# Performance work log

Measured on AMD Instinct MI355X. Metric: run time of the kernel, lower is better.

## Reference

```python
import math
import jax, jax.numpy as jnp
import numpy as np

B, T, C = 2, 2048, 1024
N_HEAD = 16
HEAD_DIM = C // N_HEAD


def setup_inputs() -> dict:
    key = jax.random.key(0)
    k1, k2, k3 = jax.random.split(key, 3)
    x = jax.random.normal(k1, (B, T, C), dtype=jnp.float32)
    w_attn = jax.random.normal(k2, (3 * C, C), dtype=jnp.float32) * 0.02
    w_proj = jax.random.normal(k3, (C, C), dtype=jnp.float32) * 0.02
    return {"x": x, "w_attn": w_attn, "w_proj": w_proj}


def _rope_cos_sin(seq_len, dim, dtype):
    inv_freq = 1.0 / (10000.0 ** (jnp.arange(0, dim, 2, dtype=jnp.float32) / dim))
    t = jnp.arange(seq_len, dtype=jnp.float32)
    freqs = jnp.einsum('i,j->ij', t, inv_freq)          # [T, dim/2]
    emb = jnp.concatenate([freqs, freqs], axis=-1)       # [T, dim]
    return jnp.cos(emb).astype(dtype), jnp.sin(emb).astype(dtype)


def _rotate_half(x):
    x1, x2 = jnp.split(x, 2, axis=-1)
    return jnp.concatenate([-x2, x1], axis=-1)


def _apply_rope(x, cos, sin):
    # x: [B, H, T, D]; cos/sin: [T, D] broadcast over batch/head
    return x * cos[None, None] + _rotate_half(x) * sin[None, None]


def reference(x, w_attn, w_proj):
    b, t, c = x.shape
    h, d = N_HEAD, c // N_HEAD
    qkv = x @ w_attn.T                                   # [B, T, 3C]
    q, k, v = jnp.split(qkv, 3, axis=-1)
    q = q.reshape(b, t, h, d).transpose(0, 2, 1, 3)      # [B, H, T, D]
    k = k.reshape(b, t, h, d).transpose(0, 2, 1, 3)
    v = v.reshape(b, t, h, d).transpose(0, 2, 1, 3)
    cos, sin = _rope_cos_sin(t, d, x.dtype)
    q = _apply_rope(q, cos, sin)
    k = _apply_rope(k, cos, sin)
    logits = jnp.einsum('bhqd,bhkd->bhqk', q, k) * (1.0 / math.sqrt(d))
    causal = jnp.tril(jnp.ones((t, t), dtype=bool))
    logits = jnp.where(causal[None, None], logits, jnp.float32(-jnp.inf).astype(logits.dtype))
    att = jax.nn.softmax(logits, axis=-1)                # [B, H, T, T]
    y = jnp.einsum('bhqk,bhkd->bhqd', att, v)            # [B, H, T, D]
    y = y.transpose(0, 2, 1, 3).reshape(b, t, c)
    return y @ w_proj.T
```

## Files before the change

kernel.cpp:

```cpp
#include <hip/hip_runtime.h>
#include <hip/hip_bf16.h>
#include <math.h>

#define B_ 2
#define T_ 2048
#define C_ 1024
#define H_ 16

typedef __bf16 bf16x8 __attribute__((ext_vector_type(8)));
typedef __bf16 bf16x4 __attribute__((ext_vector_type(4)));
typedef float f32x4 __attribute__((ext_vector_type(4)));
typedef float f32x16 __attribute__((ext_vector_type(16)));
typedef unsigned int u32;

#if __has_builtin(__builtin_amdgcn_exp2f)
#define EXP2(x) __builtin_amdgcn_exp2f(x)
#else
#define EXP2(x) exp2f(x)
#endif

__device__ __forceinline__ void gload16(const void* g, void* l) {
    __builtin_amdgcn_global_load_lds(
        (const __attribute__((address_space(1))) void*)g,
        (__attribute__((address_space(3))) void*)l, 16, 0, 0);
}

__device__ __forceinline__ f32x4 mfma16(bf16x8 a, bf16x8 b, f32x4 c) {
    return __builtin_amdgcn_mfma_f32_16x16x32_bf16(a, b, c, 0, 0, 0);
}
__device__ __forceinline__ f32x16 mfma32(bf16x8 a, bf16x8 b, f32x16 c) {
    return __builtin_amdgcn_mfma_f32_32x32x16_bf16(a, b, c, 0, 0, 0);
}

__device__ __forceinline__ u32 cvtpk(float lo, float hi) {
    u32 r;
    asm("v_cvt_pk_bf16_f32 %0, %1, %2" : "=v"(r) : "v"(lo), "v"(hi));
    return r;
}

__device__ __forceinline__ void plane32swap(u32& a, u32& b) {
#if __has_builtin(__builtin_amdgcn_permlane32_swap)
    auto r = __builtin_amdgcn_permlane32_swap(a, b, false, false);
    a = r[0]; b = r[1];
#else
    asm("v_permlane32_swap_b32 %0, %1" : "+v"(a), "+v"(b));
#endif
}

#define SCLQ 0.18033688011112042f
#define NLOG2_10K_32 (-0.4152410118609203f)

__global__ __launch_bounds__(256) void cast_all(const float* __restrict__ x,
                                                const float* __restrict__ wa,
                                                const float* __restrict__ wp,
                                                __bf16* __restrict__ xb,
                                                __bf16* __restrict__ wab,
                                                __bf16* __restrict__ wpb) {
    const int i = blockIdx.x * 256 + threadIdx.x;
    const float* src;
    __bf16* dst;
    int k;
    if (i < 1048576)               { src = x;  dst = xb;  k = i; }
    else if (i < 1048576 + 786432) { src = wa; dst = wab; k = i - 1048576; }
    else                           { src = wp; dst = wpb; k = i - (1048576 + 786432); }
    float4 v = ((const float4*)src)[k];
    bf16x4 o;
    o[0] = (__bf16)v.x; o[1] = (__bf16)v.y; o[2] = (__bf16)v.z; o[3] = (__bf16)v.w;
    ((bf16x4*)dst)[k] = o;
}

__global__ __launch_bounds__(256) void gemm_qkv(const __bf16* __restrict__ A,
                                                const __bf16* __restrict__ Bw,
                                                __bf16* __restrict__ Qb,
                                                __bf16* __restrict__ Kb,
                                                __bf16* __restrict__ Vt) {
    const int tid  = threadIdx.x;
    const int lane = tid & 63;
    const int w    = tid >> 6;
    const int wr = w >> 1, wc = w & 1;
    const int l15 = lane & 15, lg = lane >> 4;
    const int bm = blockIdx.y * 128, bn = blockIdx.x * 128;
    const int K = C_;
    __shared__ __bf16 Asm[128 * 64];
    __shared__ __bf16 Bsm[128 * 64];
    f32x4 acc[4][4] = {};

    for (int kt = 0; kt < K; kt += 64) {
        if (kt) __syncthreads();
#pragma unroll
        for (int it = 0; it < 4; ++it) {
            const int c = it * 256 + tid;
            const int row = c >> 3, cc = (c & 7) * 8;
            gload16(A  + (size_t)(bm + row) * K + kt + cc, Asm + c * 8);
            gload16(Bw + (size_t)(bn + row) * K + kt + cc, Bsm + c * 8);
        }
        __syncthreads();
#pragma unroll
        for (int kk = 0; kk < 64; kk += 32) {
            bf16x8 af[4], bf[4];
#pragma unroll
            for (int i = 0; i < 4; ++i)
                af[i] = *(const bf16x8*)&Asm[(wr * 64 + i * 16 + l15) * 64 + kk + lg * 8];
#pragma unroll
            for (int j = 0; j < 4; ++j)
                bf[j] = *(const bf16x8*)&Bsm[(wc * 64 + j * 16 + l15) * 64 + kk + lg * 8];
#pragma unroll
            for (int i = 0; i < 4; ++i)
#pragma unroll
                for (int j = 0; j < 4; ++j)
                    acc[i][j] = mfma16(af[i], bf[j], acc[i][j]);
        }
    }
    const int region  = bn >> 10;
    const int colbase = (bn & 1023) + wc * 64;
    const int h = colbase >> 6;
    if (region < 2) {
        __bf16* dst = region ? Kb : Qb;
        const float scl = region ? 1.0f : SCLQ;
#pragma unroll
        for (int j = 0; j < 2; ++j) {
            const int d = j * 16 + l15;
            const float invf = exp2f((float)d * NLOG2_10K_32);
#pragma unroll
            for (int i = 0; i < 4; ++i)
#pragma unroll
                for (int r = 0; r < 4; ++r) {
                    const int row = bm + wr * 64 + i * 16 + lg * 4 + r;
                    const int b = row >> 11, t = row & (T_ - 1);
                    float sv, cv;
                    __sincosf((float)t * invf, &sv, &cv);
                    const float v1 = acc[i][j][r], v2 = acc[i][j + 2][r];
                    const float o1 = (v1 * cv - v2 * sv) * scl;
                    const float o2 = (v2 * cv + v1 * sv) * scl;
                    const size_t base = ((size_t)(b * H_ + h) * T_ + t) * 64;
                    dst[base + d]      = (__bf16)o1;
                    dst[base + d + 32] = (__bf16)o2;
                }
        }
    } else {
#pragma unroll
        for (int i = 0; i < 4; ++i)
#pragma unroll
            for (int j = 0; j < 4; ++j) {
                const int vcol = colbase + j * 16 + l15;
                const int hh = vcol >> 6, d = vcol & 63;
                const int row0 = bm + wr * 64 + i * 16 + lg * 4;
                const int b = row0 >> 11, t0 = row0 & (T_ - 1);
                u32 dw[2];
                dw[0] = cvtpk(acc[i][j][0], acc[i][j][1]);
                dw[1] = cvtpk(acc[i][j][2], acc[i][j][3]);
                *(uint64_t*)&Vt[((size_t)(b * H_ + hh) * 64 + d) * T_ + t0] =
                    *(uint64_t*)dw;
            }
    }
}

__global__ __launch_bounds__(256) void gemm_proj(const __bf16* __restrict__ A,
                                                 const __bf16* __restrict__ Bw,
                                                 float* __restrict__ Cp,
                                                 int N, int K) {
    const int tid  = threadIdx.x;
    const int lane = tid & 63;
    const int w    = tid >> 6;
    const int wr = w >> 1, wc = w & 1;
    const int l15 = lane & 15, lg = lane >> 4;
    const int bm = blockIdx.y * 64, bn = blockIdx.x * 128;
    __shared__ __bf16 Asm[64 * 64];
    __shared__ __bf16 Bsm[128 * 64];
    f32x4 acc[2][4] = {};

    for (int kt = 0; kt < K; kt += 64) {
        if (kt) __syncthreads();
#pragma unroll
        for (int it = 0; it < 2; ++it) {
            const int g = it * 256 + tid;
            const int row = g >> 3, cc = (g & 7) * 8;
            gload16(A + (size_t)(bm + row) * K + kt + cc, Asm + g * 8);
        }
#pragma unroll
        for (int it = 0; it < 4; ++it) {
            const int g = it * 256 + tid;
            const int row = g >> 3, cc = (g & 7) * 8;
            gload16(Bw + (size_t)(bn + row) * K + kt + cc, Bsm + g * 8);
        }
        __syncthreads();
#pragma unroll
        for (int kk = 0; kk < 64; kk += 32) {
            bf16x8 af[2], bf[4];
#pragma unroll
            for (int i = 0; i < 2; ++i)
                af[i] = *(const bf16x8*)&Asm[(wr * 32 + i * 16 + l15) * 64 + kk + lg * 8];
#pragma unroll
            for (int j = 0; j < 4; ++j)
                bf[j] = *(const bf16x8*)&Bsm[(wc * 64 + j * 16 + l15) * 64 + kk + lg * 8];
#pragma unroll
            for (int i = 0; i < 2; ++i)
#pragma unroll
                for (int j = 0; j < 4; ++j)
                    acc[i][j] = mfma16(af[i], bf[j], acc[i][j]);
        }
    }
#pragma unroll
    for (int i = 0; i < 2; ++i)
#pragma unroll
        for (int j = 0; j < 4; ++j)
#pragma unroll
            for (int r = 0; r < 4; ++r) {
                const int row = bm + wr * 32 + i * 16 + lg * 4 + r;
                const int col = bn + wc * 64 + j * 16 + l15;
                Cp[(size_t)row * N + col] = acc[i][j][r];
            }
}

__global__ __launch_bounds__(256) void attn_fwd(const __bf16* __restrict__ Qb,
                                                const __bf16* __restrict__ Kb,
                                                const __bf16* __restrict__ Vt,
                                                __bf16* __restrict__ Yatt) {
    const int gid = blockIdx.x;
    const int bh = (gid & 7) * 4 + ((gid >> 3) & 3);
    const int qq = gid >> 5;
    const int qt = (qq < 8) ? (15 - qq) : (qq - 8);
    const int b = bh >> 4, h = bh & 15;
    const int tid = threadIdx.x, lane = tid & 63, w = tid >> 6;
    const int l31 = lane & 31, hi = lane >> 5;
    const int hi4 = hi * 4;
    __shared__ __bf16 Ksm[2][128 * 64];
    __shared__ __bf16 Vsm[2][64 * 128];

    const int Q0 = qt * 128 + w * 32;
    const int qg = Q0 + l31;
    const __bf16* Qp = Qb + ((size_t)bh * T_ + Q0) * 64;
    const __bf16* Kp = Kb + (size_t)bh * T_ * 64;
    const __bf16* Vp = Vt + (size_t)bh * 64 * T_;

    auto STAGE = [&](int j) {
        __bf16* Ks = Ksm[j & 1];
        __bf16* Vs = Vsm[j & 1];
#pragma unroll
        for (int it = 0; it < 4; ++it) {
            const int g = it * 256 + tid;
            const int kr = g >> 3, kc = (g & 7) ^ (kr & 7);
            gload16(Kp + ((size_t)(j * 128 + kr)) * 64 + kc * 8, Ks + g * 8);
            const int vd = g >> 4, vg = (g & 15) ^ (vd & 15);
            gload16(Vp + (size_t)vd * T_ + j * 128 + vg * 8, Vs + g * 8);
        }
    };

    const int jmax = qt + 1;
    STAGE(0);

    bf16x8 qf[4];
#pragma unroll
    for (int ds = 0; ds < 4; ++ds)
        qf[ds] = *(const bf16x8*)&Qp[l31 * 64 + ds * 16 + hi * 8];

    f32x16 ot[2] = {};
    float m_run = -1e30f, l_run = 0.f;

    for (int j = 0; j < jmax; ++j) {
        const int cur = j & 1;
        __builtin_amdgcn_s_barrier();
        if (j + 1 < jmax) {
            STAGE(j + 1);
            asm volatile("s_waitcnt vmcnt(8)" ::: "memory");
        } else {
            asm volatile("s_waitcnt vmcnt(0)" ::: "memory");
        }
        __builtin_amdgcn_s_barrier();
        __builtin_amdgcn_sched_barrier(0);

        f32x16 st[4] = {};
#pragma unroll
        for (int a = 0; a < 4; ++a)
#pragma unroll
            for (int ds = 0; ds < 4; ++ds) {
                const int row = a * 32 + l31;
                const int off = (ds * 32 + hi * 16) ^ ((row & 7) << 4);
                bf16x8 kf = *(const bf16x8*)((const char*)Ksm[cur] + row * 128 + off);
                st[a] = mfma32(kf, qf[ds], st[a]);
            }
        if (j == qt) {
#pragma unroll
            for (int a = 0; a < 4; ++a)
#pragma unroll
                for (int r = 0; r < 16; ++r) {
                    const int kv = j * 128 + a * 32 + (r & 3) + 8 * (r >> 2) + hi4;
                    if (kv > qg) st[a][r] = -1e30f;
                }
        }
        float t8[8];
#pragma unroll
        for (int i = 0; i < 8; ++i)
            t8[i] = fmaxf(fmaxf(fmaxf(st[0][i], st[0][i + 8]),
                                fmaxf(st[1][i], st[1][i + 8])),
                          fmaxf(fmaxf(st[2][i], st[2][i + 8]),
                                fmaxf(st[3][i], st[3][i + 8])));
        float mx = fmaxf(fmaxf(fmaxf(t8[0], t8[1]), fmaxf(t8[2], t8[3])),
                         fmaxf(fmaxf(t8[4], t8[5]), fmaxf(t8[6], t8[7])));
        mx = fmaxf(mx, __shfl_xor(mx, 32));
        if (!__all(mx - m_run <= 10.f)) {
            const float mnew = fmaxf(m_run, mx);
            const float corr = EXP2(m_run - mnew);
            l_run *= corr;
#pragma unroll
            for (int db = 0; db < 2; ++db)
#pragma unroll
                for (int r = 0; r < 16; ++r) ot[db][r] *= corr;
            m_run = mnew;
        }
        float s0 = 0.f, s1 = 0.f;
#pragma unroll
        for (int a = 0; a < 4; ++a)
#pragma unroll
            for (int r = 0; r < 16; ++r) {
                const float e = EXP2(st[a][r] - m_run);
                st[a][r] = e;
                if (r & 1) s1 += e; else s0 += e;
            }
        float rs = s0 + s1;
        rs += __shfl_xor(rs, 32);
        l_run += rs;
        bf16x8 pa[8];
#pragma unroll
        for (int ks = 0; ks < 8; ++ks) {
            const int a = ks >> 1, rb = (ks & 1) * 8;
            u32 X0 = cvtpk(st[a][rb + 0], st[a][rb + 1]);
            u32 X1 = cvtpk(st[a][rb + 2], st[a][rb + 3]);
            u32 Y0 = cvtpk(st[a][rb + 4], st[a][rb + 5]);
            u32 Y1 = cvtpk(st[a][rb + 6], st[a][rb + 7]);
            plane32swap(X0, Y0);
            plane32swap(X1, Y1);
            u32 dw[4] = {X0, X1, Y0, Y1};
            pa[ks] = *(bf16x8*)dw;
        }
#pragma unroll
        for (int ks = 0; ks < 8; ++ks)
#pragma unroll
            for (int db = 0; db < 2; ++db) {
                const int row = db * 32 + l31;
                const int off = ((ks * 2 + hi) ^ (row & 15)) * 16;
                bf16x8 vf = *(const bf16x8*)((const char*)Vsm[cur] + row * 256 + off);
                ot[db] = mfma32(vf, pa[ks], ot[db]);
            }
    }
    const float inv = 1.f / l_run;
    __bf16* Yp = Yatt + ((size_t)(b * T_ + qg)) * C_ + h * 64;
#pragma unroll
    for (int db = 0; db < 2; ++db)
#pragma unroll
        for (int rq = 0; rq < 4; ++rq) {
            const int r = rq * 4;
            u32 dw[2];
            dw[0] = cvtpk(ot[db][r] * inv,     ot[db][r + 1] * inv);
            dw[1] = cvtpk(ot[db][r + 2] * inv, ot[db][r + 3] * inv);
            const int d = db * 32 + 8 * rq + hi4;
            *(uint64_t*)&Yp[d] = *(uint64_t*)dw;
        }
}

extern "C" void kernel_launch(void* const* d_in, const int* in_sizes, int n_in,
                              void* d_out, int out_size, void* d_ws, size_t ws_size,
                              hipStream_t stream) {
    const float* x      = (const float*)d_in[0];
    const float* w_attn = (const float*)d_in[1];
    const float* w_proj = (const float*)d_in[2];
    float* out = (float*)d_out;
    char* ws = (char*)d_ws;

    __bf16* xb  = (__bf16*)(ws);
    __bf16* wab = (__bf16*)(ws + 8388608);
    __bf16* wpb = (__bf16*)(ws + 14680064);
    __bf16* Qb  = (__bf16*)(ws + 16777216);
    __bf16* Kb  = (__bf16*)(ws + 25165824);
    __bf16* Vt  = (__bf16*)(ws + 33554432);
    __bf16* Ya  = (__bf16*)(ws + 41943040);

    cast_all<<<dim3(8192), 256, 0, stream>>>(x, w_attn, w_proj, xb, wab, wpb);

    gemm_qkv<<<dim3(3 * C_ / 128, B_ * T_ / 128), 256, 0, stream>>>(
        xb, wab, Qb, Kb, Vt);

    attn_fwd<<<dim3(16 * 32), 256, 0, stream>>>(Qb, Kb, Vt, Ya);

    gemm_proj<<<dim3(C_ / 128, B_ * T_ / 64), 256, 0, stream>>>(
        Ya, wpb, out, C_, C_);
}
```

Measured before the change: 108.9 us.

## Rewrite QKV GEMM as 256x256 double-buffered swizzled tile kernel with priority hints

The QKV projection GEMM moves from 128x128 tiles with 4 warps and single-buffered LDS to 256x256 tiles with 8 warps. Global-to-LDS loads of the next K-step overlap the MFMA work on the current one, using 128 KB of dynamic shared memory and an XOR-swizzled layout to avoid bank conflicts. s_setprio hints are added around the MFMA blocks in both the GEMM and the attention kernel. The grid shrinks to 12x16=192 blocks, which may underfill the 256 CUs and leaves one block per CU because of the LDS size.

```diff
diff --git a/kernel.cpp b/kernel.cpp
--- a/kernel.cpp
+++ b/kernel.cpp
@@ -69,50 +69,94 @@
     ((bf16x4*)dst)[k] = o;
 }
 
-__global__ __launch_bounds__(256) void gemm_qkv(const __bf16* __restrict__ A,
-                                                const __bf16* __restrict__ Bw,
-                                                __bf16* __restrict__ Qb,
-                                                __bf16* __restrict__ Kb,
-                                                __bf16* __restrict__ Vt) {
-    const int tid  = threadIdx.x;
-    const int lane = tid & 63;
-    const int w    = tid >> 6;
-    const int wr = w >> 1, wc = w & 1;
+__global__ __launch_bounds__(512, 2) void gemm_qkv(const __bf16* __restrict__ A,
+                                                   const __bf16* __restrict__ Bw,
+                                                   __bf16* __restrict__ Qb,
+                                                   __bf16* __restrict__ Kb,
+                                                   __bf16* __restrict__ Vt) {
+    extern __shared__ __bf16 smem[];
+    __bf16* Ah = smem;
+    __bf16* Bh = smem + 2 * 2 * 128 * 64;
+    const int tid = threadIdx.x, lane = tid & 63;
+    const int w = tid >> 6, wm = w >> 2, wn = w & 3;
     const int l15 = lane & 15, lg = lane >> 4;
-    const int bm = blockIdx.y * 128, bn = blockIdx.x * 128;
+    const int bm = blockIdx.y * 256, bn = blockIdx.x * 256;
     const int K = C_;
-    __shared__ __bf16 Asm[128 * 64];
-    __shared__ __bf16 Bsm[128 * 64];
-    f32x4 acc[4][4] = {};
-
-    for (int kt = 0; kt < K; kt += 64) {
-        if (kt) __syncthreads();
-#pragma unroll
-        for (int it = 0; it < 4; ++it) {
-            const int c = it * 256 + tid;
-            const int row = c >> 3, cc = (c & 7) * 8;
-            gload16(A  + (size_t)(bm + row) * K + kt + cc, Asm + c * 8);
-            gload16(Bw + (size_t)(bn + row) * K + kt + cc, Bsm + c * 8);
-        }
-        __syncthreads();
-#pragma unroll
-        for (int kk = 0; kk < 64; kk += 32) {
-            bf16x8 af[4], bf[4];
-#pragma unroll
-            for (int i = 0; i < 4; ++i)
-                af[i] = *(const bf16x8*)&Asm[(wr * 64 + i * 16 + l15) * 64 + kk + lg * 8];
-#pragma unroll
-            for (int j = 0; j < 4; ++j)
-                bf[j] = *(const bf16x8*)&Bsm[(wc * 64 + j * 16 + l15) * 64 + kk + lg * 8];
-#pragma unroll
-            for (int i = 0; i < 4; ++i)
-#pragma unroll
-                for (int j = 0; j < 4; ++j)
-                    acc[i][j] = mfma16(af[i], bf[j], acc[i][j]);
+    f32x4 acc[8][4] = {};
+
+    auto STAGE_A = [&](int t) {
+        __bf16* dst = Ah + (t & 1) * (2 * 128 * 64);
+#pragma unroll
+        for (int q2 = 0; q2 < 4; ++q2) {
+            const int qid = q2 * 512 + tid;
+            const int half = qid >> 10;
+            const int row = (qid >> 3) & 127, g = qid & 7;
+            const int sg = g ^ (row & 7);
+            gload16(A + (size_t)(bm + half * 128 + row) * K + t * 64 + sg * 8,
+                    dst + qid * 8);
+        }
+    };
+    auto STAGE_B = [&](int t) {
+        __bf16* dst = Bh + (t & 1) * (2 * 128 * 64);
+#pragma unroll
+        for (int q2 = 0; q2 < 4; ++q2) {
+            const int qid = q2 * 512 + tid;
+            const int half = qid >> 10;
+            const int row = (qid >> 3) & 127, g = qid & 7;
+            const int sg = g ^ (row & 7);
+            gload16(Bw + (size_t)(bn + half * 128 + row) * K + t * 64 + sg * 8,
+                    dst + qid * 8);
+        }
+    };
+
+    STAGE_A(0); STAGE_B(0);
+    asm volatile("s_waitcnt vmcnt(0)" ::: "memory");
+    __builtin_amdgcn_s_barrier();
+
+    for (int t = 0; t < 16; ++t) {
+        const __bf16* As = Ah + (t & 1) * (2 * 128 * 64) + wm * (128 * 64);
+        const __bf16* Bs = Bh + (t & 1) * (2 * 128 * 64) + (wn >> 1) * (128 * 64);
+#pragma unroll
+        for (int p = 0; p < 4; ++p) {
+            const int rh = p >> 1, ch = p & 1;
+            if (p == 0 && t < 15) STAGE_A(t + 1);
+            if (p == 1 && t < 15) STAGE_B(t + 1);
+            bf16x8 af[4][2], bf[2][2];
+#pragma unroll
+            for (int i2 = 0; i2 < 4; ++i2) {
+                const int row = rh * 64 + i2 * 16 + l15;
+#pragma unroll
+                for (int k2 = 0; k2 < 2; ++k2)
+                    af[i2][k2] = *(const bf16x8*)
+                        &As[row * 64 + ((k2 * 4 + lg) ^ (row & 7)) * 8];
+            }
+#pragma unroll
+            for (int j2 = 0; j2 < 2; ++j2) {
+                const int row = (wn & 1) * 64 + ch * 32 + j2 * 16 + l15;
+#pragma unroll
+                for (int k2 = 0; k2 < 2; ++k2)
+                    bf[j2][k2] = *(const bf16x8*)
+                        &Bs[row * 64 + ((k2 * 4 + lg) ^ (row & 7)) * 8];
+            }
+            __builtin_amdgcn_s_barrier();
+            __builtin_amdgcn_s_setprio(1);
+#pragma unroll
+            for (int k2 = 0; k2 < 2; ++k2)
+#pragma unroll
+                for (int i2 = 0; i2 < 4; ++i2)
+#pragma unroll
+                    for (int j2 = 0; j2 < 2; ++j2)
+                        acc[rh * 4 + i2][ch * 2 + j2] =
+                            mfma16(af[i2][k2], bf[j2][k2],
+                                   acc[rh * 4 + i2][ch * 2 + j2]);
+            __builtin_amdgcn_s_setprio(0);
+            if (p == 3) asm volatile("s_waitcnt vmcnt(0)" ::: "memory");
+            __builtin_amdgcn_s_barrier();
         }
     }
-    const int region  = bn >> 10;
-    const int colbase = (bn & 1023) + wc * 64;
+    const int cb = bn + wn * 64;
+    const int region = cb >> 10;
+    const int colbase = cb & 1023;
     const int h = colbase >> 6;
     if (region < 2) {
         __bf16* dst = region ? Kb : Qb;
@@ -122,33 +166,33 @@
             const int d = j * 16 + l15;
             const float invf = exp2f((float)d * NLOG2_10K_32);
 #pragma unroll
-            for (int i = 0; i < 4; ++i)
+            for (int i = 0; i < 8; ++i)
 #pragma unroll
                 for (int r = 0; r < 4; ++r) {
-                    const int row = bm + wr * 64 + i * 16 + lg * 4 + r;
-                    const int b = row >> 11, t = row & (T_ - 1);
+                    const int row = bm + wm * 128 + i * 16 + lg * 4 + r;
+                    const int b = row >> 11, tt = row & (T_ - 1);
                     float sv, cv;
-                    __sincosf((float)t * invf, &sv, &cv);
+                    __sincosf((float)tt * invf, &sv, &cv);
                     const float v1 = acc[i][j][r], v2 = acc[i][j + 2][r];
                     const float o1 = (v1 * cv - v2 * sv) * scl;
                     const float o2 = (v2 * cv + v1 * sv) * scl;
-                    const size_t base = ((size_t)(b * H_ + h) * T_ + t) * 64;
+                    const size_t base = ((size_t)(b * H_ + h) * T_ + tt) * 64;
                     dst[base + d]      = (__bf16)o1;
                     dst[base + d + 32] = (__bf16)o2;
                 }
         }
     } else {
 #pragma unroll
-        for (int i = 0; i < 4; ++i)
-#pragma unroll
-            for (int j = 0; j < 4; ++j) {
-                const int vcol = colbase + j * 16 + l15;
+        for (int i = 0; i < 8; ++i)
+#pragma unroll
+            for (int jj = 0; jj < 4; ++jj) {
+                const int vcol = colbase + jj * 16 + l15;
                 const int hh = vcol >> 6, d = vcol & 63;
-                const int row0 = bm + wr * 64 + i * 16 + lg * 4;
+                const int row0 = bm + wm * 128 + i * 16 + lg * 4;
                 const int b = row0 >> 11, t0 = row0 & (T_ - 1);
                 u32 dw[2];
-                dw[0] = cvtpk(acc[i][j][0], acc[i][j][1]);
-                dw[1] = cvtpk(acc[i][j][2], acc[i][j][3]);
+                dw[0] = cvtpk(acc[i][jj][0], acc[i][jj][1]);
+                dw[1] = cvtpk(acc[i][jj][2], acc[i][jj][3]);
                 *(uint64_t*)&Vt[((size_t)(b * H_ + hh) * 64 + d) * T_ + t0] =
                     *(uint64_t*)dw;
             }
@@ -270,6 +314,7 @@
         __builtin_amdgcn_sched_barrier(0);
 
         f32x16 st[4] = {};
+        __builtin_amdgcn_s_setprio(1);
 #pragma unroll
         for (int a = 0; a < 4; ++a)
 #pragma unroll
@@ -279,6 +324,7 @@
                 bf16x8 kf = *(const bf16x8*)((const char*)Ksm[cur] + row * 128 + off);
                 st[a] = mfma32(kf, qf[ds], st[a]);
             }
+        __builtin_amdgcn_s_setprio(0);
         if (j == qt) {
 #pragma unroll
             for (int a = 0; a < 4; ++a)
@@ -333,6 +379,7 @@
             u32 dw[4] = {X0, X1, Y0, Y1};
             pa[ks] = *(bf16x8*)dw;
         }
+        __builtin_amdgcn_s_setprio(1);
 #pragma unroll
         for (int ks = 0; ks < 8; ++ks)
 #pragma unroll
@@ -342,6 +389,7 @@
                 bf16x8 vf = *(const bf16x8*)((const char*)Vsm[cur] + row * 256 + off);
                 ot[db] = mfma32(vf, pa[ks], ot[db]);
             }
+        __builtin_amdgcn_s_setprio(0);
     }
     const float inv = 1.f / l_run;
     __bf16* Yp = Yatt + ((size_t)(b * T_ + qg)) * C_ + h * 64;
@@ -377,7 +425,7 @@
 
     cast_all<<<dim3(8192), 256, 0, stream>>>(x, w_attn, w_proj, xb, wab, wpb);
 
-    gemm_qkv<<<dim3(3 * C_ / 128, B_ * T_ / 128), 256, 0, stream>>>(
+    gemm_qkv<<<dim3(3 * C_ / 256, B_ * T_ / 256), 512, 131072, stream>>>(
         xb, wab, Qb, Kb, Vt);
 
     attn_fwd<<<dim3(16 * 32), 256, 0, stream>>>(Qb, Kb, Vt, Ya);
```

After: 115.0 us. 5.6% more time.
